# Performance work log

Hardware: AMD Instinct MI355X
Metric: run time of the kernel (lower is better)

Reference implementation:

```python
import jax, jax.numpy as jnp
import numpy as np

B, N, H, D, MAXH, MRP = 64, 197, 12, 64, 16, 14  # batch, tokens (14x14+cls), heads, head_dim, supernet max heads, max rel pos
TABLE = 2 * MRP + 2  # 30 rows per table


def setup_inputs() -> dict:
    key = jax.random.key(0)
    ks = jax.random.split(key, 5)
    x = jax.random.normal(ks[0], (B, N, 3 * D * MAXH), dtype=jnp.float32)
    mk = lambda k: (0.02 * jax.random.normal(k, (TABLE, D), dtype=jnp.float32))
    return {"x": x, "tk_v": mk(ks[1]), "tk_h": mk(ks[2]), "tv_v": mk(ks[3]), "tv_h": mk(ks[4])}


def _rel_pos_emb(table_v, table_h, n):
    # RelativePosition2D_super.forward(length_q=n, length_k=n)
    lq = n - 1
    s = int(np.sqrt(lq))  # 14
    r = jnp.arange(lq)
    dv = r[None, :] // s - r[:, None] // s
    dh = r[None, :] % s - r[:, None] % s
    iv = jnp.clip(dv, -MRP, MRP) + MRP + 1
    ih = jnp.clip(dh, -MRP, MRP) + MRP + 1
    iv = jnp.pad(iv, ((1, 0), (1, 0)))  # CLS row/col -> index 0
    ih = jnp.pad(ih, ((1, 0), (1, 0)))
    return table_v[iv] + table_h[ih]  # (n, n, D)


def reference(x, tk_v, tk_h, tv_v, tv_h):
    scale = D ** (-0.5)  # sample_scale = 64**-0.5
    xs = x[:, :, : H * D * 3]
    qkv = xs.reshape(B, N, 3, H, D).transpose(2, 0, 3, 1, 4)  # (3,B,H,N,D)
    q, k, v = qkv[0], qkv[1], qkv[2]
    attn = jnp.einsum('bhid,bhjd->bhij', q, k) * scale
    rk = _rel_pos_emb(tk_v, tk_h, N)  # (N,N,D)
    attn = attn + jnp.einsum('bhid,ijd->bhij', q, rk) * scale
    attn = jax.nn.softmax(attn, axis=-1)  # attn_drop p=0.0 -> identity
    out = jnp.einsum('bhij,bhjd->bhid', attn, v)
    rv = _rel_pos_emb(tv_v, tv_h, N)  # (N,N,D)
    out = out + jnp.einsum('bhij,ijd->bhid', attn, rv)
    out = out.transpose(0, 2, 1, 3).reshape(B, N, H * D)  # (B,N,768)
    return jnp.pad(out, ((0, 0), (0, 0), (0, MAXH * D - H * D)))  # pad to (B,N,1024)
```

## Files before the change

### kernel.cpp

```cpp
#include <hip/hip_runtime.h>

typedef float  f4v   __attribute__((ext_vector_type(4)));
typedef float  f32x4 __attribute__((ext_vector_type(4)));
typedef short  s8v   __attribute__((ext_vector_type(8)));
typedef short  s4v   __attribute__((ext_vector_type(4)));
typedef __bf16 bf16x8 __attribute__((ext_vector_type(8)));

#define N_   197
#define H_   12
#define CIN  3072
#define COUT 1024
#define VSTR 296
#define ASTR 72
#define BSTR 40

#define MEMBAR() asm volatile("" ::: "memory")

__device__ __forceinline__ unsigned short f2bf(float f) {
    unsigned u = __float_as_uint(f);
    u += 0x7FFFu + ((u >> 16) & 1u);
    return (unsigned short)(u >> 16);
}
__device__ __forceinline__ float bf2f(unsigned short s) {
    return __uint_as_float(((unsigned)s) << 16);
}
__device__ __forceinline__ f32x4 mfma_bf16(s8v a, s8v b, f32x4 c) {
    return __builtin_amdgcn_mfma_f32_16x16x32_bf16(
        __builtin_bit_cast(bf16x8, a), __builtin_bit_cast(bf16x8, b), c, 0, 0, 0);
}
__device__ __forceinline__ void st4f(volatile unsigned short* p, float a, float b, float c, float d) {
    s4v v;
    v[0] = (short)f2bf(a); v[1] = (short)f2bf(b);
    v[2] = (short)f2bf(c); v[3] = (short)f2bf(d);
    *(volatile s4v*)p = v;
}
__device__ __forceinline__ void st4z(volatile unsigned short* p) {
    s4v v = {0, 0, 0, 0};
    *(volatile s4v*)p = v;
}

__launch_bounds__(1024, 4)
__global__ void attn_super(const float* __restrict__ x,
                           const float* __restrict__ tkv,
                           const float* __restrict__ tkh,
                           const float* __restrict__ tvv,
                           const float* __restrict__ tvh,
                           float* __restrict__ out) {
    __shared__ __align__(16) unsigned short Kl[272 * 72];
    __shared__ __align__(16) unsigned short Vt[64 * VSTR];
    __shared__ __align__(16) unsigned short AR[16][16 * ASTR];
    __shared__ __align__(16) unsigned short INDv[16 * 224];
    __shared__ __align__(16) unsigned short INDh[16 * 224];
    __shared__ __align__(16) unsigned short Bext[224 * BSTR];

    const int bid = blockIdx.x;
    const int b = bid / H_, h = bid % H_;
    const int tid = threadIdx.x;
    const int w  = tid >> 6;
    const int l  = tid & 63;
    const int lg = l >> 4;
    const int ln = l & 15;

    const float* xb = x + (size_t)b * N_ * CIN;

    if (h < 4) {
        float* oz = out + (size_t)b * N_ * COUT + 768 + h * 64;
        for (int idx = tid; idx < N_ * 16; idx += 1024) {
            int row = idx >> 4, c4 = idx & 15;
            f4v z = {0.f, 0.f, 0.f, 0.f};
            *(f4v*)(oz + (size_t)row * COUT + c4 * 4) = z;
        }
    }

    f4v kr[5];
    #pragma unroll
    for (int it = 0; it < 5; ++it) {
        int idx = it * 1024 + tid;
        bool a5 = (it < 4) || (tid < 256);
        int row = idx >> 4, d0 = (idx & 15) * 4;
        f4v v = {0.f, 0.f, 0.f, 0.f};
        if (a5) {
            if (row < N_)                     v = *(const f4v*)(xb + (size_t)row * CIN + 768 + h * 64 + d0);
            else if (row >= 208 && row < 238) v = *(const f4v*)(tkv + (row - 208) * 64 + d0);
            else if (row >= 240 && row < 270) v = *(const f4v*)(tkh + (row - 240) * 64 + d0);
        }
        kr[it] = v;
    }
    f4v q1[2], q2[2];
    if (w < 13) {
        int qrow = w * 16 + ln; if (qrow > 196) qrow = 196;
        const float* qp = xb + (size_t)qrow * CIN + h * 64;
        #pragma unroll
        for (int s2 = 0; s2 < 2; ++s2) {
            q1[s2] = *(const f4v*)(qp + s2 * 32 + lg * 8);
            q2[s2] = *(const f4v*)(qp + s2 * 32 + lg * 8 + 4);
        }
    }
    f4v vr[5];
    #pragma unroll
    for (int it = 0; it < 5; ++it) {
        int idx = it * 1024 + tid;
        bool a5 = (it < 4) || (tid < 512);
        int j = idx % 288, d0 = (idx / 288) * 4;
        f4v v = {0.f, 0.f, 0.f, 0.f};
        if (a5) {
            if (j < N_)                     v = *(const f4v*)(xb + (size_t)j * CIN + 1536 + h * 64 + d0);
            else if (j >= 224 && j < 254)   v = *(const f4v*)(tvv + (j - 224) * 64 + d0);
            else if (j >= 256 && j < 286)   v = *(const f4v*)(tvh + (j - 256) * 64 + d0);
        }
        vr[it] = v;
    }

    #pragma unroll
    for (int it = 0; it < 5; ++it) {
        int idx = it * 1024 + tid;
        bool a5 = (it < 4) || (tid < 256);
        if (a5) {
            int row = idx >> 4, d0 = (idx & 15) * 4;
            f4v v = kr[it];
            s4v pk;
            pk[0] = (short)f2bf(v[0]); pk[1] = (short)f2bf(v[1]);
            pk[2] = (short)f2bf(v[2]); pk[3] = (short)f2bf(v[3]);
            *(s4v*)(&Kl[row * 72 + d0]) = pk;
        }
    }
    for (int idx = tid; idx < 16 * 224; idx += 1024) {
        int m = idx / 224, k = idx % 224;
        int km1 = k - 1;
        bool kv = (k >= 1 && k <= 196);
        INDv[idx] = (kv && (km1 / 14) == m) ? (unsigned short)0x3F80 : (unsigned short)0;
        INDh[idx] = (kv && (km1 % 14) == m) ? (unsigned short)0x3F80 : (unsigned short)0;
    }
    for (int idx = tid; idx < 224 * 32; idx += 1024) {
        int k = idx >> 5, c = idx & 31;
        unsigned short v = 0;
        if (k >= 1 && k <= 196) {
            int mj = (k - 1) / 14, cj = (k - 1) - mj * 14;
            if (c == mj || c == 16 + cj) v = (unsigned short)0x3F80;
        } else if (k == 0) {
            if (c == 15 || c == 31) v = (unsigned short)0x3F80;
        }
        Bext[k * BSTR + c] = v;
    }
    __syncthreads();

    const int tile = w, qb = tile * 16;
    const unsigned short* ar = &AR[w][0];
    volatile unsigned short* arv = &AR[w][0];

    f32x4 S[13];
    float rsq[4], p0q[4];
    int ritq[4], citq[4];
    if (w < 13) {
        const int iL  = qb + ln;
        const int im1 = (iL > 0) ? iL - 1 : 0;
        const int rit = im1 / 14;
        const int cit = im1 - rit * 14;

        s8v aq[2];
        #pragma unroll
        for (int s2 = 0; s2 < 2; ++s2) {
            #pragma unroll
            for (int e = 0; e < 4; ++e) {
                aq[s2][e]     = (short)f2bf(q1[s2][e] * 0.125f);
                aq[s2][e + 4] = (short)f2bf(q2[s2][e] * 0.125f);
            }
        }
        float spv = 0.f, sph = 0.f;
        #pragma unroll
        for (int tt = 0; tt < 4; ++tt) {
            f32x4 acc = {0.f, 0.f, 0.f, 0.f};
            #pragma unroll
            for (int s2 = 0; s2 < 2; ++s2) {
                const s8v bk = *(const s8v*)(&Kl[((13 + tt) * 16 + ln) * 72 + s2 * 32 + lg * 8]);
                acc = mfma_bf16(bk, aq[s2], acc);
            }
            const bool isV  = (tt < 2);
            const int mbase = (tt & 1) * 16;
            const int shift = isV ? rit : cit;
            const int cbase = isV ? 0 : 16;
            const bool skip0 = (tile == 0 && ln == 0);
            #pragma unroll
            for (int r = 0; r < 4; ++r) {
                int m = mbase + 4 * lg + r;
                int t = m + shift - 15;
                if (!skip0 && m < 30 && t >= 0 && t < 15)
                    arv[ln * ASTR + cbase + t] = f2bf(acc[r]);
                if (!skip0 && m == 0)
                    arv[ln * ASTR + cbase + 15] = f2bf(acc[r]);
            }
            if (tile == 0 && l == 0) {
                if (tt == 0) spv = acc[0];
                if (tt == 2) sph = acc[0];
            }
        }
        if (tile == 0 && l == 0) {
            unsigned short v0 = f2bf(spv), h0 = f2bf(sph);
            #pragma unroll
            for (int t = 0; t < 16; ++t) {
                arv[t] = v0;
                arv[16 + t] = h0;
            }
        }
        MEMBAR();
        const s8v aq2 = *(const s8v*)(&ar[ln * ASTR + lg * 8]);
        #pragma unroll
        for (int ct = 0; ct < 13; ++ct) {
            const s8v be = *(const s8v*)(&Bext[(ct * 16 + ln) * BSTR + lg * 8]);
            f32x4 acc = {0.f, 0.f, 0.f, 0.f};
            acc = mfma_bf16(be, aq2, acc);
            #pragma unroll
            for (int s2 = 0; s2 < 2; ++s2) {
                const s8v bk = *(const s8v*)(&Kl[(ct * 16 + ln) * 72 + s2 * 32 + lg * 8]);
                acc = mfma_bf16(bk, aq[s2], acc);
            }
            S[ct] = acc;
        }
    }
    #pragma unroll
    for (int it = 0; it < 5; ++it) {
        int idx = it * 1024 + tid;
        bool a5 = (it < 4) || (tid < 512);
        if (a5) {
            int j = idx % 288, d0 = (idx / 288) * 4;
            f4v v = vr[it];
            #pragma unroll
            for (int e = 0; e < 4; ++e)
                Vt[(d0 + e) * VSTR + j] = f2bf(v[e]);
        }
    }

    if (w < 13) {
        float rs4[4] = {0.f, 0.f, 0.f, 0.f};
        #pragma unroll
        for (int ct = 0; ct < 13; ++ct) {
            #pragma unroll
            for (int r = 0; r < 4; ++r) {
                float p = __expf(S[ct][r]);
                if (ct == 12) { if (4 * lg + r > 4) p = 0.f; }
                S[ct][r] = p;
                rs4[r] += p;
            }
        }
        float rs = (rs4[0] + rs4[1]) + (rs4[2] + rs4[3]);
        rs += __shfl_xor(rs, 16);
        rs += __shfl_xor(rs, 32);
        float p00 = S[0][0];
        #pragma unroll
        for (int r = 0; r < 4; ++r) {
            rsq[r] = __shfl(rs,  4 * lg + r);
            p0q[r] = __shfl(p00, 4 * lg + r);
        }
        #pragma unroll
        for (int r = 0; r < 4; ++r) {
            int qr2 = qb + 4 * lg + r;
            int im  = (qr2 > 0) ? qr2 - 1 : 0;
            ritq[r] = im / 14;
            citq[r] = im - ritq[r] * 14;
        }
    }
    __syncthreads();

    if (w >= 13) return;

    f32x4 oacc[4];
    #pragma unroll
    for (int nt = 0; nt < 4; ++nt) { f32x4 z = {0.f,0.f,0.f,0.f}; oacc[nt] = z; }
    f32x4 cwv = {0.f,0.f,0.f,0.f}, cwh = {0.f,0.f,0.f,0.f};

    #pragma unroll
    for (int win = 0; win < 3; ++win) {
        MEMBAR();
        #pragma unroll
        for (int cc = 0; cc < 4; ++cc) {
            int ct = win * 4 + cc;
            st4f(&arv[ln * ASTR + cc * 16 + 4 * lg], S[ct][0], S[ct][1], S[ct][2], S[ct][3]);
        }
        MEMBAR();
        #pragma unroll
        for (int kk = 0; kk < 2; ++kk) {
            int kt = win * 2 + kk;
            const s8v ap = *(const s8v*)(&ar[ln * ASTR + kk * 32 + lg * 8]);
            #pragma unroll
            for (int nt = 0; nt < 4; ++nt) {
                const s8v bv = *(const s8v*)(&Vt[(nt * 16 + ln) * VSTR + kt * 32 + lg * 8]);
                oacc[nt] = mfma_bf16(ap, bv, oacc[nt]);
            }
            const s8v bi = *(const s8v*)(&INDv[ln * 224 + kt * 32 + lg * 8]);
            cwv = mfma_bf16(ap, bi, cwv);
            const s8v bh = *(const s8v*)(&INDh[ln * 224 + kt * 32 + lg * 8]);
            cwh = mfma_bf16(ap, bh, cwh);
        }
    }
    {
        MEMBAR();
        st4f(&arv[ln * ASTR + 4 * lg], S[12][0], S[12][1], S[12][2], S[12][3]);
        st4z(&arv[ln * ASTR + 16 + 4 * lg]);
        st4z(&arv[ln * ASTR + 32 + lg * 8]);
        st4z(&arv[ln * ASTR + 36 + lg * 8]);
        MEMBAR();
        {
            const s8v ap = *(const s8v*)(&ar[ln * ASTR + lg * 8]);
            #pragma unroll
            for (int nt = 0; nt < 4; ++nt) {
                const s8v bv = *(const s8v*)(&Vt[(nt * 16 + ln) * VSTR + 192 + lg * 8]);
                oacc[nt] = mfma_bf16(ap, bv, oacc[nt]);
            }
            const s8v bi = *(const s8v*)(&INDv[ln * 224 + 192 + lg * 8]);
            cwv = mfma_bf16(ap, bi, cwv);
            const s8v bh = *(const s8v*)(&INDh[ln * 224 + 192 + lg * 8]);
            cwh = mfma_bf16(ap, bh, cwh);
        }
        MEMBAR();
        #pragma unroll
        for (int r = 0; r < 4; ++r) {
            int q = 4 * lg + r;
            bool isRow0 = (tile == 0) && (q == 0);
            if (ln <= 13 && !isRow0)
                arv[q * ASTR + 47 + ln - ritq[r]] = f2bf(cwv[r]);
            if (ln == 15)
                arv[q * ASTR + 32] = f2bf(isRow0 ? rsq[r] : p0q[r]);
        }
        MEMBAR();
        {
            const s8v ap = *(const s8v*)(&ar[ln * ASTR + 32 + lg * 8]);
            #pragma unroll
            for (int nt = 0; nt < 4; ++nt) {
                const s8v bv = *(const s8v*)(&Vt[(nt * 16 + ln) * VSTR + 224 + lg * 8]);
                oacc[nt] = mfma_bf16(ap, bv, oacc[nt]);
            }
        }
    }
    {
        MEMBAR();
        st4z(&arv[ln * ASTR + lg * 8]);
        st4z(&arv[ln * ASTR + 4 + lg * 8]);
        MEMBAR();
        #pragma unroll
        for (int r = 0; r < 4; ++r) {
            int q = 4 * lg + r;
            bool isRow0 = (tile == 0) && (q == 0);
            if (ln <= 13 && !isRow0)
                arv[q * ASTR + 15 + ln - citq[r]] = f2bf(cwh[r]);
            if (ln == 15)
                arv[q * ASTR + 0] = f2bf(isRow0 ? rsq[r] : p0q[r]);
        }
        MEMBAR();
        {
            const s8v ap = *(const s8v*)(&ar[ln * ASTR + lg * 8]);
            #pragma unroll
            for (int nt = 0; nt < 4; ++nt) {
                const s8v bv = *(const s8v*)(&Vt[(nt * 16 + ln) * VSTR + 256 + lg * 8]);
                oacc[nt] = mfma_bf16(ap, bv, oacc[nt]);
            }
        }
    }
    #pragma unroll
    for (int r = 0; r < 4; ++r) {
        int n = qb + 4 * lg + r;
        if (n < N_) {
            float sc = 1.0f / rsq[r];
            float* orow = out + ((size_t)b * N_ + n) * COUT + h * 64;
            #pragma unroll
            for (int nt = 0; nt < 4; ++nt)
                orow[nt * 16 + ln] = oacc[nt][r] * sc;
        }
    }
}

extern "C" void kernel_launch(void* const* d_in, const int* in_sizes, int n_in,
                              void* d_out, int out_size, void* d_ws, size_t ws_size,
                              hipStream_t stream) {
    const float* x   = (const float*)d_in[0];
    const float* tkv = (const float*)d_in[1];
    const float* tkh = (const float*)d_in[2];
    const float* tvv = (const float*)d_in[3];
    const float* tvh = (const float*)d_in[4];
    float* o = (float*)d_out;
    attn_super<<<dim3(64 * H_), dim3(1024), 0, stream>>>(x, tkv, tkh, tvv, tvh, o);
}
```

Measured before the change: 71.65 us.

## Precompute indicator tables in a separate kernel and add MFMA wave priority

```diff
diff --git a/kernel.cpp b/kernel.cpp
--- a/kernel.cpp
+++ b/kernel.cpp
@@ -13,6 +13,9 @@
 #define VSTR 296
 #define ASTR 72
 #define BSTR 40
+#define G_INDV 8960
+#define G_INDH 12544
+#define TABSZ  16128
 
 #define MEMBAR() asm volatile("" ::: "memory")
 
@@ -20,9 +23,6 @@
     unsigned u = __float_as_uint(f);
     u += 0x7FFFu + ((u >> 16) & 1u);
     return (unsigned short)(u >> 16);
-}
-__device__ __forceinline__ float bf2f(unsigned short s) {
-    return __uint_as_float(((unsigned)s) << 16);
 }
 __device__ __forceinline__ f32x4 mfma_bf16(s8v a, s8v b, f32x4 c) {
     return __builtin_amdgcn_mfma_f32_16x16x32_bf16(
@@ -37,6 +37,34 @@
 __device__ __forceinline__ void st4z(volatile unsigned short* p) {
     s4v v = {0, 0, 0, 0};
     *(volatile s4v*)p = v;
+}
+
+__global__ void init_tabs(unsigned short* __restrict__ g) {
+    int idx = blockIdx.x * 256 + threadIdx.x;
+    if (idx >= TABSZ) return;
+    unsigned short v = 0;
+    if (idx < G_INDV) {
+        int k = idx / 40, c = idx - k * 40;
+        if (c < 32) {
+            if (k >= 1 && k <= 196) {
+                int mj = (k - 1) / 14, cj = (k - 1) - mj * 14;
+                if (c == mj || c == 16 + cj) v = (unsigned short)0x3F80;
+            } else if (k == 0) {
+                if (c == 15 || c == 31) v = (unsigned short)0x3F80;
+            }
+        }
+    } else {
+        int t = idx - G_INDV;
+        int tab = t / 3584;
+        int r = t - tab * 3584;
+        int m = r / 224, k = r - m * 224;
+        if (k >= 1 && k <= 196) {
+            int km1 = k - 1;
+            int mk = tab ? (km1 % 14) : (km1 / 14);
+            if (mk == m) v = (unsigned short)0x3F80;
+        }
+    }
+    g[idx] = v;
 }
 
 __launch_bounds__(1024, 4)
@@ -45,13 +73,16 @@
                            const float* __restrict__ tkh,
                            const float* __restrict__ tvv,
                            const float* __restrict__ tvh,
+                           const unsigned short* __restrict__ gt,
                            float* __restrict__ out) {
     __shared__ __align__(16) unsigned short Kl[272 * 72];
     __shared__ __align__(16) unsigned short Vt[64 * VSTR];
     __shared__ __align__(16) unsigned short AR[16][16 * ASTR];
-    __shared__ __align__(16) unsigned short INDv[16 * 224];
-    __shared__ __align__(16) unsigned short INDh[16 * 224];
-    __shared__ __align__(16) unsigned short Bext[224 * BSTR];
+    __shared__ __align__(16) unsigned short TAB[TABSZ];
+
+    const unsigned short* Bext = TAB;
+    const unsigned short* INDv = TAB + G_INDV;
+    const unsigned short* INDh = TAB + G_INDH;
 
     const int bid = blockIdx.x;
     const int b = bid / H_, h = bid % H_;
@@ -109,6 +140,10 @@
             else if (j >= 256 && j < 286)   v = *(const f4v*)(tvh + (j - 256) * 64 + d0);
         }
         vr[it] = v;
+    }
+    for (int idx = tid; idx < TABSZ / 8; idx += 1024) {
+        const s8v tv = *(const s8v*)(&gt[idx * 8]);
+        *(s8v*)(&TAB[idx * 8]) = tv;
     }
 
     #pragma unroll
@@ -124,24 +159,6 @@
             *(s4v*)(&Kl[row * 72 + d0]) = pk;
         }
     }
-    for (int idx = tid; idx < 16 * 224; idx += 1024) {
-        int m = idx / 224, k = idx % 224;
-        int km1 = k - 1;
-        bool kv = (k >= 1 && k <= 196);
-        INDv[idx] = (kv && (km1 / 14) == m) ? (unsigned short)0x3F80 : (unsigned short)0;
-        INDh[idx] = (kv && (km1 % 14) == m) ? (unsigned short)0x3F80 : (unsigned short)0;
-    }
-    for (int idx = tid; idx < 224 * 32; idx += 1024) {
-        int k = idx >> 5, c = idx & 31;
-        unsigned short v = 0;
-        if (k >= 1 && k <= 196) {
-            int mj = (k - 1) / 14, cj = (k - 1) - mj * 14;
-            if (c == mj || c == 16 + cj) v = (unsigned short)0x3F80;
-        } else if (k == 0) {
-            if (c == 15 || c == 31) v = (unsigned short)0x3F80;
-        }
-        Bext[k * BSTR + c] = v;
-    }
     __syncthreads();
 
     const int tile = w, qb = tile * 16;
@@ -204,6 +221,7 @@
         }
         MEMBAR();
         const s8v aq2 = *(const s8v*)(&ar[ln * ASTR + lg * 8]);
+        __builtin_amdgcn_s_setprio(1);
         #pragma unroll
         for (int ct = 0; ct < 13; ++ct) {
             const s8v be = *(const s8v*)(&Bext[(ct * 16 + ln) * BSTR + lg * 8]);
@@ -216,6 +234,7 @@
             }
             S[ct] = acc;
         }
+        __builtin_amdgcn_s_setprio(0);
     }
     #pragma unroll
     for (int it = 0; it < 5; ++it) {
@@ -268,6 +287,7 @@
     for (int nt = 0; nt < 4; ++nt) { f32x4 z = {0.f,0.f,0.f,0.f}; oacc[nt] = z; }
     f32x4 cwv = {0.f,0.f,0.f,0.f}, cwh = {0.f,0.f,0.f,0.f};
 
+    __builtin_amdgcn_s_setprio(1);
     #pragma unroll
     for (int win = 0; win < 3; ++win) {
         MEMBAR();
@@ -355,6 +375,7 @@
             }
         }
     }
+    __builtin_amdgcn_s_setprio(0);
     #pragma unroll
     for (int r = 0; r < 4; ++r) {
         int n = qb + 4 * lg + r;
@@ -377,5 +398,7 @@
     const float* tvv = (const float*)d_in[3];
     const float* tvh = (const float*)d_in[4];
     float* o = (float*)d_out;
-    attn_super<<<dim3(64 * H_), dim3(1024), 0, stream>>>(x, tkv, tkh, tvv, tvh, o);
-}
+    unsigned short* gt = (unsigned short*)d_ws;
+    init_tabs<<<dim3(63), dim3(256), 0, stream>>>(gt);
+    attn_super<<<dim3(64 * H_), dim3(1024), 0, stream>>>(x, tkv, tkh, tvv, tvh, gt, o);
+}
```

Result: slower. 74.73 us (+4.3%).
